# Kernel tuning notes

Hardware: AMD Instinct MI355X
Metric: run time of the kernel (lower is better)

The kernel has to match this reference:

```python
import jax, jax.numpy as jnp
import numpy as np

B, S, DIM, HID, E, TOPK = 32, 512, 1024, 4096, 8, 2
CF = 1.0


def setup_inputs() -> dict:
    key = jax.random.key(0)
    ks = jax.random.split(key, 12)
    sc = 0.02
    return {
        "router_input": jax.random.normal(ks[0], (B, S, DIM), jnp.float32),
        "x": jax.random.normal(ks[1], (B, S, DIM), jnp.float32),
        "noise": jax.random.normal(ks[2], (B, E), jnp.float32),
        # router params (stored [in,out])
        "Wg": jax.random.normal(ks[3], (DIM, E), jnp.float32) * sc,
        "bg": jnp.zeros((E,), jnp.float32),
        "Wn": jax.random.normal(ks[4], (DIM, E), jnp.float32) * sc,
        "bn": jnp.zeros((E,), jnp.float32),
        # expert MLP params, stacked over experts
        "W1": jax.random.normal(ks[5], (E, DIM, HID), jnp.float32) * sc,
        "b1": jnp.zeros((E, HID), jnp.float32),
        "W2": jax.random.normal(ks[6], (E, HID, DIM), jnp.float32) * sc,
        "b2": jnp.zeros((E, DIM), jnp.float32),
    }


def reference(router_input, x, noise, Wg, bg, Wn, bn, W1, b1, W2, b2):
    b, s, d = x.shape
    e = Wg.shape[1]
    # ---- noisy top-k router (per-sample: mean over sequence) ----
    ri = router_input.mean(axis=1)                      # [B, D]
    logits = ri @ Wg + bg                               # [B, E]
    noise_logits = ri @ Wn + bn                         # [B, E]
    noisy = logits + noise * jax.nn.softplus(noise_logits)
    top_vals, top_idx = jax.lax.top_k(noisy, TOPK)      # [B, K]
    # softmax over -inf-masked logits == softmax over the kept top-k values
    gate = jax.nn.softmax(top_vals, axis=-1)            # [B, K]

    flat_e = top_idx.reshape(-1)                        # [N] expert id per (sample,k) pair
    flat_w = gate.reshape(-1)                           # [N]
    sample_ids = jnp.repeat(jnp.arange(b), TOPK)        # [N]
    n = b * TOPK
    capacity = max(int(n / e * CF), 1)

    # ---- capacity drop: keep first `capacity` pairs per expert in sorted order ----
    order = jnp.argsort(flat_e, stable=True)            # stable sort by expert id
    sorted_e = flat_e[order]
    rank_in_expert = jnp.arange(n) - jnp.searchsorted(sorted_e, sorted_e, side="left")
    keep = jnp.zeros((n,), bool).at[order].set(rank_in_expert < capacity)

    # ---- per-pair expert MLP via gathered expert weights (grouped GEMM) ----
    xp = x[sample_ids]                                  # [N, S, D]
    h = jnp.einsum("psd,pdh->psh", xp, W1[flat_e]) + b1[flat_e][:, None, :]
    h = jax.nn.gelu(h, approximate=False)               # exact GELU (torch nn.GELU)
    y = jnp.einsum("psh,phd->psd", h, W2[flat_e]) + b2[flat_e][:, None, :]

    # ---- weight by gate, zero dropped pairs, combine back per sample ----
    y = y * (flat_w * keep.astype(y.dtype))[:, None, None]
    return jax.ops.segment_sum(y, sample_ids, num_segments=b)  # [B, S, D]
```

## Files before the change

kernel.cpp:

```cpp
#include <hip/hip_runtime.h>
#include <hip/hip_bf16.h>
#include <math.h>

#define B_    32
#define S_    512
#define DIM_  1024
#define HID_  4096
#define E_    8
#define TOPK_ 2
#define CAP_  8
#define NSLOT_ 64

typedef __bf16 bf16_t;
typedef bf16_t bf16x8 __attribute__((ext_vector_type(8)));
typedef float  f32x4  __attribute__((ext_vector_type(4)));

__device__ __forceinline__ ushort f2bf(float f) {
    union { float f; unsigned u; } v; v.f = f;
    unsigned r = (v.u + 0x7fffu + ((v.u >> 16) & 1u)) >> 16;
    return (ushort)r;
}

__device__ __forceinline__ void async_cp16(const ushort* g, ushort* l) {
    __builtin_amdgcn_global_load_lds(
        (const __attribute__((address_space(1))) unsigned int*)g,
        (__attribute__((address_space(3))) unsigned int*)l, 16, 0, 0);
}

__global__ void k_mean_p(const float* __restrict__ rin, float* __restrict__ part) {
    int p = blockIdx.x, b = blockIdx.y;
    int d4 = threadIdx.x;
    const float4* base = (const float4*)(rin + ((size_t)b * S_ + p * 32) * DIM_) + d4;
    float4 acc = {0.f, 0.f, 0.f, 0.f};
    for (int s = 0; s < 32; ++s) {
        float4 v = base[(size_t)s * (DIM_ / 4)];
        acc.x += v.x; acc.y += v.y; acc.z += v.z; acc.w += v.w;
    }
    ((float4*)(part + (size_t)(b * 16 + p) * DIM_))[d4] = acc;
}

__global__ void k_mean_f(const float* __restrict__ part, float* __restrict__ ri) {
    int b = blockIdx.x, d4 = threadIdx.x;
    float4 acc = {0.f, 0.f, 0.f, 0.f};
    for (int p = 0; p < 16; ++p) {
        float4 v = ((const float4*)(part + (size_t)(b * 16 + p) * DIM_))[d4];
        acc.x += v.x; acc.y += v.y; acc.z += v.z; acc.w += v.w;
    }
    const float inv = 1.0f / (float)S_;
    float4 o = {acc.x * inv, acc.y * inv, acc.z * inv, acc.w * inv};
    ((float4*)(ri + (size_t)b * DIM_))[d4] = o;
}

__global__ void k_router_logits(const float* __restrict__ ri, const float* __restrict__ noise,
                                const float* __restrict__ Wg, const float* __restrict__ bg,
                                const float* __restrict__ Wn, const float* __restrict__ bn,
                                float* __restrict__ noisy) {
    __shared__ float rrow[DIM_];
    __shared__ float pg[256], pn[256];
    int b = blockIdx.x, t = threadIdx.x;
    ((float4*)rrow)[t] = ((const float4*)(ri + (size_t)b * DIM_))[t];
    __syncthreads();
    int e = t & 7, c = t >> 3;
    float ag = 0.f, an = 0.f;
    for (int i = 0; i < 32; ++i) {
        float rv = rrow[c * 32 + i];
        ag += rv * Wg[(c * 32 + i) * E_ + e];
        an += rv * Wn[(c * 32 + i) * E_ + e];
    }
    pg[t] = ag; pn[t] = an;
    __syncthreads();
    for (int off = 128; off >= 8; off >>= 1) {
        if (t < off) { pg[t] += pg[t + off]; pn[t] += pn[t + off]; }
        __syncthreads();
    }
    if (t < E_) {
        float lg = pg[t] + bg[t];
        float ln = pn[t] + bn[t];
        float sp = (ln > 20.f) ? ln : log1pf(expf(ln));
        noisy[b * E_ + t] = lg + noise[b * E_ + t] * sp;
    }
}

__global__ void k_router_assign(const float* __restrict__ noisy,
                                int* __restrict__ slot_sample, float* __restrict__ slot_gate,
                                int* __restrict__ sample_slot, float* __restrict__ sample_gate) {
    __shared__ int   top_i[B_][TOPK_];
    __shared__ float top_g[B_][TOPK_];
    int t = threadIdx.x;
    if (t < B_) {
        float v1 = -INFINITY, v2 = -INFINITY; int i1 = 0, i2 = 0;
        for (int ee = 0; ee < E_; ++ee) {
            float v = noisy[t * E_ + ee];
            if (v > v1)      { v2 = v1; i2 = i1; v1 = v; i1 = ee; }
            else if (v > v2) { v2 = v; i2 = ee; }
        }
        float g2 = expf(v2 - v1);
        float s = 1.f + g2;
        top_i[t][0] = i1; top_i[t][1] = i2;
        top_g[t][0] = 1.f / s; top_g[t][1] = g2 / s;
    }
    if (t < NSLOT_)      { slot_sample[t] = -1; slot_gate[t] = 0.f; }
    if (t < B_ * TOPK_)  { sample_slot[t] = -1; sample_gate[t] = 0.f; }
    __syncthreads();
    if (t == 0) {
        int cnt[E_];
        for (int ee = 0; ee < E_; ++ee) cnt[ee] = 0;
        for (int p = 0; p < B_ * TOPK_; ++p) {
            int bb = p >> 1, kk = p & 1;
            int ee = top_i[bb][kk];
            int c = cnt[ee]++;
            if (c < CAP_) {
                int slot = ee * CAP_ + c;
                slot_sample[slot] = bb;
                slot_gate[slot]   = top_g[bb][kk];
                sample_slot[bb * TOPK_ + kk] = slot;
                sample_gate[bb * TOPK_ + kk] = top_g[bb][kk];
            }
        }
    }
}

__global__ void k_cvt_x(const float* __restrict__ x, ushort* __restrict__ xb, int n8) {
    int i = blockIdx.x * blockDim.x + threadIdx.x;
    if (i >= n8) return;
    const float4* p = (const float4*)x + (size_t)i * 2;
    float4 a = p[0], b = p[1];
    union { ushort s[8]; uint4 v; } u;
    u.s[0] = f2bf(a.x); u.s[1] = f2bf(a.y); u.s[2] = f2bf(a.z); u.s[3] = f2bf(a.w);
    u.s[4] = f2bf(b.x); u.s[5] = f2bf(b.y); u.s[6] = f2bf(b.z); u.s[7] = f2bf(b.w);
    ((uint4*)xb)[i] = u.v;
}

__global__ void k_transpose_cvt(const float* __restrict__ W, ushort* __restrict__ Wt,
                                int K, int N) {
    __shared__ float tile[64][65];
    size_t eoff = (size_t)blockIdx.z * K * N;
    const float* Win = W + eoff;
    ushort* Wout = Wt + eoff;
    int n0 = blockIdx.x * 64, k0 = blockIdx.y * 64;
    int t = threadIdx.x;
    int r = t >> 4;
    int c4 = (t & 15) << 2;
#pragma unroll
    for (int i = 0; i < 4; ++i) {
        float4 v = *(const float4*)(Win + (size_t)(k0 + r + i * 16) * N + n0 + c4);
        tile[r + i * 16][c4 + 0] = v.x;
        tile[r + i * 16][c4 + 1] = v.y;
        tile[r + i * 16][c4 + 2] = v.z;
        tile[r + i * 16][c4 + 3] = v.w;
    }
    __syncthreads();
#pragma unroll
    for (int i = 0; i < 4; ++i) {
        int nn = r + i * 16;
        ushort4 o;
        o.x = f2bf(tile[c4 + 0][nn]);
        o.y = f2bf(tile[c4 + 1][nn]);
        o.z = f2bf(tile[c4 + 2][nn]);
        o.w = f2bf(tile[c4 + 3][nn]);
        *(ushort4*)(Wout + (size_t)(n0 + nn) * K + k0 + c4) = o;
    }
}

__device__ __forceinline__ void gemm_mainloop(
    const ushort* __restrict__ Abase, int lda,
    const ushort* __restrict__ Bbase, int ldb,
    int K, ushort* lds_a, ushort* lds_b, f32x4 acc[4][4]) {
    int tid = threadIdx.x;
    int wave = tid >> 6, lane = tid & 63;
    int wm = wave & 1, wn = wave >> 1;
    int quad = lane >> 4, mr = lane & 15;
    int r_lo = lane >> 2;
    int kp   = (lane & 3) << 3;
    const ushort* a_g0 = Abase + (size_t)(wave * 16 + r_lo) * lda + kp;
    const ushort* a_g1 = Abase + (size_t)((wave + 4) * 16 + r_lo) * lda + kp;
    const ushort* b_g0 = Bbase + (size_t)(wave * 16 + r_lo) * ldb + kp;
    const ushort* b_g1 = Bbase + (size_t)((wave + 4) * 16 + r_lo) * ldb + kp;
    ushort* a_l0 = lds_a + wave * 512;
    ushort* a_l1 = lds_a + (wave + 4) * 512;
    ushort* b_l0 = lds_b + wave * 512;
    ushort* b_l1 = lds_b + (wave + 4) * 512;
    for (int k0 = 0; k0 < K; k0 += 32) {
        __syncthreads();
        async_cp16(a_g0 + k0, a_l0);
        async_cp16(a_g1 + k0, a_l1);
        async_cp16(b_g0 + k0, b_l0);
        async_cp16(b_g1 + k0, b_l1);
        __syncthreads();
        bf16x8 af[4], bfr[4];
#pragma unroll
        for (int i = 0; i < 4; ++i)
            af[i] = *(const bf16x8*)&lds_a[(wm * 64 + i * 16 + mr) * 32 + quad * 8];
#pragma unroll
        for (int i = 0; i < 4; ++i)
            bfr[i] = *(const bf16x8*)&lds_b[(wn * 64 + i * 16 + mr) * 32 + quad * 8];
#pragma unroll
        for (int i = 0; i < 4; ++i)
#pragma unroll
            for (int j = 0; j < 4; ++j)
                acc[i][j] = __builtin_amdgcn_mfma_f32_16x16x32_bf16(af[i], bfr[j], acc[i][j], 0, 0, 0);
    }
}

__global__ __launch_bounds__(256, 2) void k_gemm1(
    const ushort* __restrict__ xb, const ushort* __restrict__ w1t,
    const float* __restrict__ b1, const int* __restrict__ slot_sample,
    ushort* __restrict__ H) {
    __shared__ ushort As[128 * 32];
    __shared__ ushort Bs[128 * 32];
    int slot = blockIdx.z;
    int samp = slot_sample[slot];
    if (samp < 0) return;
    int e = slot >> 3;
    int mt = blockIdx.y, nt = blockIdx.x;
    const ushort* Abase = xb + ((size_t)samp * S_ + mt * 128) * DIM_;
    const ushort* Bbase = w1t + (size_t)e * HID_ * DIM_ + (size_t)(nt * 128) * DIM_;
    f32x4 acc[4][4];
#pragma unroll
    for (int i = 0; i < 4; ++i)
#pragma unroll
        for (int j = 0; j < 4; ++j) acc[i][j] = (f32x4){0.f, 0.f, 0.f, 0.f};
    gemm_mainloop(Abase, DIM_, Bbase, DIM_, DIM_, As, Bs, acc);
    int wave = threadIdx.x >> 6, lane = threadIdx.x & 63;
    int wm = wave & 1, wn = wave >> 1, quad = lane >> 4, mr = lane & 15;
    ushort* Hrow = H + ((size_t)slot * S_ + mt * 128) * HID_ + nt * 128;
#pragma unroll
    for (int j = 0; j < 4; ++j) {
        int nl = wn * 64 + j * 16 + mr;
        float bias = b1[e * HID_ + nt * 128 + nl];
#pragma unroll
        for (int i = 0; i < 4; ++i) {
#pragma unroll
            for (int r = 0; r < 4; ++r) {
                int ml = wm * 64 + i * 16 + quad * 4 + r;
                float v = acc[i][j][r] + bias;
                float g = 0.5f * v * (1.0f + erff(v * 0.70710678118654752f));
                Hrow[(size_t)ml * HID_ + nl] = f2bf(g);
            }
        }
    }
}

__global__ __launch_bounds__(256, 2) void k_gemm2(
    const ushort* __restrict__ H, const ushort* __restrict__ w2t,
    const float* __restrict__ b2, const int* __restrict__ sample_slot,
    const float* __restrict__ sample_gate, float* __restrict__ out) {
    __shared__ ushort As[128 * 32];
    __shared__ ushort Bs[128 * 32];
    int b = blockIdx.z;
    int sl0 = sample_slot[b * TOPK_ + 0], sl1 = sample_slot[b * TOPK_ + 1];
    float ga0 = sample_gate[b * TOPK_ + 0], ga1 = sample_gate[b * TOPK_ + 1];
    if (sl0 < 0) { sl0 = sl1; ga0 = ga1; sl1 = -1; }
    int mt = blockIdx.y, nt = blockIdx.x;
    f32x4 acc[4][4];
#pragma unroll
    for (int i = 0; i < 4; ++i)
#pragma unroll
        for (int j = 0; j < 4; ++j) acc[i][j] = (f32x4){0.f, 0.f, 0.f, 0.f};
    if (sl0 >= 0) {
        int e0 = sl0 >> 3;
        gemm_mainloop(H + ((size_t)sl0 * S_ + mt * 128) * HID_, HID_,
                      w2t + (size_t)e0 * DIM_ * HID_ + (size_t)(nt * 128) * HID_, HID_,
                      HID_, As, Bs, acc);
    }
    if (sl1 >= 0) {
        float ratio = ga0 / ga1;
#pragma unroll
        for (int i = 0; i < 4; ++i)
#pragma unroll
            for (int j = 0; j < 4; ++j) acc[i][j] = acc[i][j] * ratio;
        int e1 = sl1 >> 3;
        gemm_mainloop(H + ((size_t)sl1 * S_ + mt * 128) * HID_, HID_,
                      w2t + (size_t)e1 * DIM_ * HID_ + (size_t)(nt * 128) * HID_, HID_,
                      HID_, As, Bs, acc);
    }
    float gfin = (sl1 >= 0) ? ga1 : ((sl0 >= 0) ? ga0 : 0.f);
    int wave = threadIdx.x >> 6, lane = threadIdx.x & 63;
    int wm = wave & 1, wn = wave >> 1, quad = lane >> 4, mr = lane & 15;
    float* Orow = out + ((size_t)b * S_ + mt * 128) * DIM_ + nt * 128;
#pragma unroll
    for (int j = 0; j < 4; ++j) {
        int nl = wn * 64 + j * 16 + mr;
        float bias = 0.f;
        if (sl0 >= 0) bias += ga0 * b2[(sl0 >> 3) * DIM_ + nt * 128 + nl];
        if (sl1 >= 0) bias += ga1 * b2[(sl1 >> 3) * DIM_ + nt * 128 + nl];
#pragma unroll
        for (int i = 0; i < 4; ++i) {
#pragma unroll
            for (int r = 0; r < 4; ++r) {
                int ml = wm * 64 + i * 16 + quad * 4 + r;
                Orow[(size_t)ml * DIM_ + nl] = acc[i][j][r] * gfin + bias;
            }
        }
    }
}

extern "C" void kernel_launch(void* const* d_in, const int* in_sizes, int n_in,
                              void* d_out, int out_size, void* d_ws, size_t ws_size,
                              hipStream_t stream) {
    const float* rin   = (const float*)d_in[0];
    const float* x     = (const float*)d_in[1];
    const float* noise = (const float*)d_in[2];
    const float* Wg    = (const float*)d_in[3];
    const float* bg    = (const float*)d_in[4];
    const float* Wn    = (const float*)d_in[5];
    const float* bn    = (const float*)d_in[6];
    const float* W1    = (const float*)d_in[7];
    const float* b1    = (const float*)d_in[8];
    const float* W2    = (const float*)d_in[9];
    const float* b2    = (const float*)d_in[10];
    float* out = (float*)d_out;

    char* ws = (char*)d_ws;
    float*  ri          = (float*)ws;
    int*    slot_sample = (int*)(ws + 131072);
    float*  slot_gate   = (float*)(ws + 131328);
    int*    sample_slot = (int*)(ws + 131584);
    float*  sample_gate = (float*)(ws + 131840);
    ushort* xb  = (ushort*)(ws + 135168);
    ushort* w1t = (ushort*)(ws + 135168 + 33554432);
    ushort* w2t = (ushort*)(ws + 135168 + 33554432 + 67108864);
    ushort* H   = (ushort*)(ws + 135168 + 33554432 + 2 * 67108864);
    float* part  = (float*)H;
    float* noisy = (float*)((char*)H + 2097152);

    k_mean_p<<<dim3(16, B_), 256, 0, stream>>>(rin, part);
    k_mean_f<<<B_, 256, 0, stream>>>(part, ri);
    k_router_logits<<<B_, 256, 0, stream>>>(ri, noise, Wg, bg, Wn, bn, noisy);
    k_router_assign<<<1, 256, 0, stream>>>(noisy, slot_sample, slot_gate,
                                           sample_slot, sample_gate);
    k_cvt_x<<<(B_ * S_ * DIM_ / 8 + 255) / 256, 256, 0, stream>>>(x, xb, B_ * S_ * DIM_ / 8);
    k_transpose_cvt<<<dim3(HID_ / 64, DIM_ / 64, E_), 256, 0, stream>>>(W1, w1t, DIM_, HID_);
    k_transpose_cvt<<<dim3(DIM_ / 64, HID_ / 64, E_), 256, 0, stream>>>(W2, w2t, HID_, DIM_);
    k_gemm1<<<dim3(HID_ / 128, S_ / 128, NSLOT_), 256, 0, stream>>>(xb, w1t, b1, slot_sample, H);
    k_gemm2<<<dim3(DIM_ / 128, S_ / 128, B_), 256, 0, stream>>>(H, w2t, b2, sample_slot,
                                                                sample_gate, out);
}
```

Baseline: 1.137 ms.

## Use 256x256 tiles with swizzled multi-stage LDS pipeline in expert GEMMs

Both expert GEMMs move from 128x128 tiles with 256 threads to 256x256 tiles with 512 threads. The new main loop keeps a 4-slot LDS ring with loads issued two steps ahead, an XOR-swizzled LDS layout to avoid bank conflicts, split A/B staging interleaved with MFMA, and raised wave priority during MFMA. A flattened grid maps blocks in groups of eight for better L2 locality. The larger tiles cut global and LDS traffic per FLOP, but they use 128KB of LDS per block and many accumulator registers, and leave fewer blocks (256 in gemm2) to fill the CUs.

```diff
diff --git a/kernel.cpp b/kernel.cpp
--- a/kernel.cpp
+++ b/kernel.cpp
@@ -162,133 +162,180 @@
     }
 }
 
-__device__ __forceinline__ void gemm_mainloop(
+__device__ __forceinline__ void gemm_mainloop256(
     const ushort* __restrict__ Abase, int lda,
     const ushort* __restrict__ Bbase, int ldb,
-    int K, ushort* lds_a, ushort* lds_b, f32x4 acc[4][4]) {
-    int tid = threadIdx.x;
-    int wave = tid >> 6, lane = tid & 63;
-    int wm = wave & 1, wn = wave >> 1;
-    int quad = lane >> 4, mr = lane & 15;
-    int r_lo = lane >> 2;
-    int kp   = (lane & 3) << 3;
-    const ushort* a_g0 = Abase + (size_t)(wave * 16 + r_lo) * lda + kp;
-    const ushort* a_g1 = Abase + (size_t)((wave + 4) * 16 + r_lo) * lda + kp;
-    const ushort* b_g0 = Bbase + (size_t)(wave * 16 + r_lo) * ldb + kp;
-    const ushort* b_g1 = Bbase + (size_t)((wave + 4) * 16 + r_lo) * ldb + kp;
-    ushort* a_l0 = lds_a + wave * 512;
-    ushort* a_l1 = lds_a + (wave + 4) * 512;
-    ushort* b_l0 = lds_b + wave * 512;
-    ushort* b_l1 = lds_b + (wave + 4) * 512;
-    for (int k0 = 0; k0 < K; k0 += 32) {
-        __syncthreads();
-        async_cp16(a_g0 + k0, a_l0);
-        async_cp16(a_g1 + k0, a_l1);
-        async_cp16(b_g0 + k0, b_l0);
-        async_cp16(b_g1 + k0, b_l1);
-        __syncthreads();
-        bf16x8 af[4], bfr[4];
+    int K, ushort* lds, f32x4 acc[8][4]) {
+    const int tid  = threadIdx.x;
+    const int wave = tid >> 6, lane = tid & 63;
+    const int wm = wave >> 2, wn = wave & 3;
+    const int quad = lane >> 4, mr = lane & 15;
+    const int nt = K >> 5;
+    const unsigned swz = (((unsigned)(mr & 3)) << 4) | (((unsigned)((mr >> 2) & 1)) << 6);
+    unsigned offA[8], offB[4];
+#pragma unroll
+    for (int i = 0; i < 8; ++i)
+        offA[i] = (((unsigned)(wm * 128 + i * 16 + mr) * 64u + (unsigned)quad * 16u) ^ swz);
+#pragma unroll
+    for (int j = 0; j < 4; ++j)
+        offB[j] = 16384u + (((unsigned)(wn * 64 + j * 16 + mr) * 64u + (unsigned)quad * 16u) ^ swz);
+    int srow[2], squad[2];
+    unsigned sldso[2];
+#pragma unroll
+    for (int h = 0; h < 2; ++h) {
+        unsigned tt = (unsigned)(2 * wave + h) * 1024u + (unsigned)lane * 16u;
+        int row = (int)(((tt >> 7) << 1) | (((tt >> 6) & 1u) ^ ((tt >> 8) & 1u)));
+        int q   = (int)(((tt >> 4) & 3u) ^ (unsigned)(row & 3));
+        srow[h] = row; squad[h] = q;
+        sldso[h] = (unsigned)(2 * wave + h) * 1024u;
+    }
+    const ushort* gA0 = Abase + (size_t)srow[0] * lda + squad[0] * 8;
+    const ushort* gA1 = Abase + (size_t)srow[1] * lda + squad[1] * 8;
+    const ushort* gB0 = Bbase + (size_t)srow[0] * ldb + squad[0] * 8;
+    const ushort* gB1 = Bbase + (size_t)srow[1] * ldb + squad[1] * 8;
+    char* ldsb = (char*)lds;
+#define STAGE_A_(tt_) do { \
+        char* s_ = ldsb + ((tt_) & 3) * 32768; int k0_ = (tt_) * 32; \
+        async_cp16(gA0 + k0_, (ushort*)(s_ + sldso[0])); \
+        async_cp16(gA1 + k0_, (ushort*)(s_ + sldso[1])); } while (0)
+#define STAGE_B_(tt_) do { \
+        char* s_ = ldsb + ((tt_) & 3) * 32768 + 16384; int k0_ = (tt_) * 32; \
+        async_cp16(gB0 + k0_, (ushort*)(s_ + sldso[0])); \
+        async_cp16(gB1 + k0_, (ushort*)(s_ + sldso[1])); } while (0)
+    STAGE_A_(0); STAGE_B_(0); STAGE_A_(1); STAGE_B_(1);
+    asm volatile("s_waitcnt vmcnt(4)" ::: "memory");
+    __builtin_amdgcn_s_barrier();
+    for (int t = 0; t < nt; ++t) {
+        const char* sb = ldsb + (t & 3) * 32768;
+        bf16x8 a[4], b[4];
+#pragma unroll
+        for (int i = 0; i < 4; ++i) a[i] = *(const bf16x8*)(sb + offA[i]);
+#pragma unroll
+        for (int j = 0; j < 4; ++j) b[j] = *(const bf16x8*)(sb + offB[j]);
+        if (t + 2 < nt) STAGE_A_(t + 2);
+        __builtin_amdgcn_s_barrier();
+        asm volatile("s_waitcnt lgkmcnt(0)" ::: "memory");
+        __builtin_amdgcn_sched_barrier(0);
+        __builtin_amdgcn_s_setprio(1);
 #pragma unroll
         for (int i = 0; i < 4; ++i)
-            af[i] = *(const bf16x8*)&lds_a[(wm * 64 + i * 16 + mr) * 32 + quad * 8];
+#pragma unroll
+            for (int j = 0; j < 4; ++j)
+                acc[i][j] = __builtin_amdgcn_mfma_f32_16x16x32_bf16(a[i], b[j], acc[i][j], 0, 0, 0);
+        __builtin_amdgcn_s_setprio(0);
+        __builtin_amdgcn_s_barrier();
+#pragma unroll
+        for (int i = 0; i < 4; ++i) a[i] = *(const bf16x8*)(sb + offA[4 + i]);
+        if (t + 2 < nt) STAGE_B_(t + 2);
+        __builtin_amdgcn_s_barrier();
+        asm volatile("s_waitcnt lgkmcnt(0)" ::: "memory");
+        __builtin_amdgcn_sched_barrier(0);
+        __builtin_amdgcn_s_setprio(1);
 #pragma unroll
         for (int i = 0; i < 4; ++i)
-            bfr[i] = *(const bf16x8*)&lds_b[(wn * 64 + i * 16 + mr) * 32 + quad * 8];
-#pragma unroll
-        for (int i = 0; i < 4; ++i)
 #pragma unroll
             for (int j = 0; j < 4; ++j)
-                acc[i][j] = __builtin_amdgcn_mfma_f32_16x16x32_bf16(af[i], bfr[j], acc[i][j], 0, 0, 0);
-    }
-}
-
-__global__ __launch_bounds__(256, 2) void k_gemm1(
+                acc[4 + i][j] = __builtin_amdgcn_mfma_f32_16x16x32_bf16(a[i], b[j], acc[4 + i][j], 0, 0, 0);
+        __builtin_amdgcn_s_setprio(0);
+        if (t + 2 < nt)      { asm volatile("s_waitcnt vmcnt(4)" ::: "memory"); }
+        else if (t + 1 < nt) { asm volatile("s_waitcnt vmcnt(0)" ::: "memory"); }
+        __builtin_amdgcn_s_barrier();
+    }
+#undef STAGE_A_
+#undef STAGE_B_
+}
+
+__global__ __launch_bounds__(512, 2) void k_gemm1(
     const ushort* __restrict__ xb, const ushort* __restrict__ w1t,
     const float* __restrict__ b1, const int* __restrict__ slot_sample,
     ushort* __restrict__ H) {
-    __shared__ ushort As[128 * 32];
-    __shared__ ushort Bs[128 * 32];
-    int slot = blockIdx.z;
+    __shared__ __attribute__((aligned(16))) ushort lds[65536];
+    unsigned F = blockIdx.x;
+    int low3 = F & 7; unsigned rest = F >> 3;
+    int nt_ = rest & 15; int g = rest >> 4;
+    int u1 = g * 8 + low3;
+    int slot = u1 >> 1, mt = u1 & 1;
     int samp = slot_sample[slot];
     if (samp < 0) return;
     int e = slot >> 3;
-    int mt = blockIdx.y, nt = blockIdx.x;
-    const ushort* Abase = xb + ((size_t)samp * S_ + mt * 128) * DIM_;
-    const ushort* Bbase = w1t + (size_t)e * HID_ * DIM_ + (size_t)(nt * 128) * DIM_;
-    f32x4 acc[4][4];
-#pragma unroll
-    for (int i = 0; i < 4; ++i)
+    const ushort* Abase = xb + ((size_t)samp * S_ + mt * 256) * DIM_;
+    const ushort* Bbase = w1t + (size_t)e * HID_ * DIM_ + (size_t)(nt_ * 256) * DIM_;
+    f32x4 acc[8][4];
+#pragma unroll
+    for (int i = 0; i < 8; ++i)
 #pragma unroll
         for (int j = 0; j < 4; ++j) acc[i][j] = (f32x4){0.f, 0.f, 0.f, 0.f};
-    gemm_mainloop(Abase, DIM_, Bbase, DIM_, DIM_, As, Bs, acc);
+    gemm_mainloop256(Abase, DIM_, Bbase, DIM_, DIM_, lds, acc);
     int wave = threadIdx.x >> 6, lane = threadIdx.x & 63;
-    int wm = wave & 1, wn = wave >> 1, quad = lane >> 4, mr = lane & 15;
-    ushort* Hrow = H + ((size_t)slot * S_ + mt * 128) * HID_ + nt * 128;
+    int wm = wave >> 2, wn = wave & 3, quad = lane >> 4, mr = lane & 15;
+    ushort* Hrow = H + ((size_t)slot * S_ + mt * 256) * HID_ + nt_ * 256;
 #pragma unroll
     for (int j = 0; j < 4; ++j) {
         int nl = wn * 64 + j * 16 + mr;
-        float bias = b1[e * HID_ + nt * 128 + nl];
-#pragma unroll
-        for (int i = 0; i < 4; ++i) {
+        float bias = b1[e * HID_ + nt_ * 256 + nl];
+#pragma unroll
+        for (int i = 0; i < 8; ++i) {
 #pragma unroll
             for (int r = 0; r < 4; ++r) {
-                int ml = wm * 64 + i * 16 + quad * 4 + r;
+                int ml = wm * 128 + i * 16 + quad * 4 + r;
                 float v = acc[i][j][r] + bias;
-                float g = 0.5f * v * (1.0f + erff(v * 0.70710678118654752f));
-                Hrow[(size_t)ml * HID_ + nl] = f2bf(g);
+                float gl = 0.5f * v * (1.0f + erff(v * 0.70710678118654752f));
+                Hrow[(size_t)ml * HID_ + nl] = f2bf(gl);
             }
         }
     }
 }
 
-__global__ __launch_bounds__(256, 2) void k_gemm2(
+__global__ __launch_bounds__(512, 2) void k_gemm2(
     const ushort* __restrict__ H, const ushort* __restrict__ w2t,
     const float* __restrict__ b2, const int* __restrict__ sample_slot,
     const float* __restrict__ sample_gate, float* __restrict__ out) {
-    __shared__ ushort As[128 * 32];
-    __shared__ ushort Bs[128 * 32];
-    int b = blockIdx.z;
+    __shared__ __attribute__((aligned(16))) ushort lds[65536];
+    unsigned F = blockIdx.x;
+    int low3 = F & 7; unsigned rest = F >> 3;
+    int nt_ = rest & 3; int g = rest >> 2;
+    int u = g * 8 + low3;
+    int b = u >> 1, mt = u & 1;
     int sl0 = sample_slot[b * TOPK_ + 0], sl1 = sample_slot[b * TOPK_ + 1];
     float ga0 = sample_gate[b * TOPK_ + 0], ga1 = sample_gate[b * TOPK_ + 1];
     if (sl0 < 0) { sl0 = sl1; ga0 = ga1; sl1 = -1; }
-    int mt = blockIdx.y, nt = blockIdx.x;
-    f32x4 acc[4][4];
-#pragma unroll
-    for (int i = 0; i < 4; ++i)
+    f32x4 acc[8][4];
+#pragma unroll
+    for (int i = 0; i < 8; ++i)
 #pragma unroll
         for (int j = 0; j < 4; ++j) acc[i][j] = (f32x4){0.f, 0.f, 0.f, 0.f};
     if (sl0 >= 0) {
         int e0 = sl0 >> 3;
-        gemm_mainloop(H + ((size_t)sl0 * S_ + mt * 128) * HID_, HID_,
-                      w2t + (size_t)e0 * DIM_ * HID_ + (size_t)(nt * 128) * HID_, HID_,
-                      HID_, As, Bs, acc);
+        gemm_mainloop256(H + ((size_t)sl0 * S_ + mt * 256) * HID_, HID_,
+                         w2t + (size_t)e0 * DIM_ * HID_ + (size_t)(nt_ * 256) * HID_, HID_,
+                         HID_, lds, acc);
     }
     if (sl1 >= 0) {
         float ratio = ga0 / ga1;
 #pragma unroll
-        for (int i = 0; i < 4; ++i)
+        for (int i = 0; i < 8; ++i)
 #pragma unroll
             for (int j = 0; j < 4; ++j) acc[i][j] = acc[i][j] * ratio;
         int e1 = sl1 >> 3;
-        gemm_mainloop(H + ((size_t)sl1 * S_ + mt * 128) * HID_, HID_,
-                      w2t + (size_t)e1 * DIM_ * HID_ + (size_t)(nt * 128) * HID_, HID_,
-                      HID_, As, Bs, acc);
+        gemm_mainloop256(H + ((size_t)sl1 * S_ + mt * 256) * HID_, HID_,
+                         w2t + (size_t)e1 * DIM_ * HID_ + (size_t)(nt_ * 256) * HID_, HID_,
+                         HID_, lds, acc);
     }
     float gfin = (sl1 >= 0) ? ga1 : ((sl0 >= 0) ? ga0 : 0.f);
     int wave = threadIdx.x >> 6, lane = threadIdx.x & 63;
-    int wm = wave & 1, wn = wave >> 1, quad = lane >> 4, mr = lane & 15;
-    float* Orow = out + ((size_t)b * S_ + mt * 128) * DIM_ + nt * 128;
+    int wm = wave >> 2, wn = wave & 3, quad = lane >> 4, mr = lane & 15;
+    float* Orow = out + ((size_t)b * S_ + mt * 256) * DIM_ + nt_ * 256;
 #pragma unroll
     for (int j = 0; j < 4; ++j) {
         int nl = wn * 64 + j * 16 + mr;
         float bias = 0.f;
-        if (sl0 >= 0) bias += ga0 * b2[(sl0 >> 3) * DIM_ + nt * 128 + nl];
-        if (sl1 >= 0) bias += ga1 * b2[(sl1 >> 3) * DIM_ + nt * 128 + nl];
-#pragma unroll
-        for (int i = 0; i < 4; ++i) {
+        if (sl0 >= 0) bias += ga0 * b2[(sl0 >> 3) * DIM_ + nt_ * 256 + nl];
+        if (sl1 >= 0) bias += ga1 * b2[(sl1 >> 3) * DIM_ + nt_ * 256 + nl];
+#pragma unroll
+        for (int i = 0; i < 8; ++i) {
 #pragma unroll
             for (int r = 0; r < 4; ++r) {
-                int ml = wm * 64 + i * 16 + quad * 4 + r;
+                int ml = wm * 128 + i * 16 + quad * 4 + r;
                 Orow[(size_t)ml * DIM_ + nl] = acc[i][j][r] * gfin + bias;
             }
         }
@@ -332,7 +379,6 @@
     k_cvt_x<<<(B_ * S_ * DIM_ / 8 + 255) / 256, 256, 0, stream>>>(x, xb, B_ * S_ * DIM_ / 8);
     k_transpose_cvt<<<dim3(HID_ / 64, DIM_ / 64, E_), 256, 0, stream>>>(W1, w1t, DIM_, HID_);
     k_transpose_cvt<<<dim3(DIM_ / 64, HID_ / 64, E_), 256, 0, stream>>>(W2, w2t, HID_, DIM_);
-    k_gemm1<<<dim3(HID_ / 128, S_ / 128, NSLOT_), 256, 0, stream>>>(xb, w1t, b1, slot_sample, H);
-    k_gemm2<<<dim3(DIM_ / 128, S_ / 128, B_), 256, 0, stream>>>(H, w2t, b2, sample_slot,
-                                                                sample_gate, out);
-}
+    k_gemm1<<<128 * 16, 512, 0, stream>>>(xb, w1t, b1, slot_sample, H);
+    k_gemm2<<<64 * 4, 512, 0, stream>>>(H, w2t, b2, sample_slot, sample_gate, out);
+}
```

Result: faster. 1.067 ms (-6.1%).
